# Kernel tuning notes

Hardware: AMD Instinct MI355X
Metric: run time of the kernel (lower is better)

The kernel has to match this reference:

```python
import jax, jax.numpy as jnp
import numpy as np

B, L, D, H, M = 4, 2048, 256, 8, 256
HEAD = D // H
EPS = 1e-6


def _pos_embedding(maxlen, d):
    i = np.arange(maxlen, dtype=np.float64)[:, None]
    j = np.arange(d, dtype=np.float64)[None, :]
    angle = i / np.power(10000.0, (j - (j % 2)) / d)
    pe = np.where(j % 2 == 0, np.sin(angle), np.cos(angle))
    return jnp.asarray(pe, jnp.float32)  # [L, D]


def _projection_matrix(m, d, seed=0):
    # FAVOR+ orthogonal random features: one full QR block (m == d here),
    # rows rescaled by norms of iid Gaussian rows (scaling=0 in source).
    rng = np.random.default_rng(seed)
    block = rng.standard_normal((d, d))
    q, _ = np.linalg.qr(block)
    q = q.T[:m]
    mult = np.linalg.norm(rng.standard_normal((m, d)), axis=1)
    return jnp.asarray(mult[:, None] * q, jnp.float32)  # [M, D]


def _softmax_kernel(x, is_query, proj):
    # x: [B, L, H, D], proj: [M, D]
    d = x.shape[-1]
    m = proj.shape[0]
    x = x * (float(d) ** -0.25)
    xp = jnp.einsum('blhd,md->blhm', x, proj)
    diag = 0.5 * jnp.sum(x * x, axis=-1, keepdims=True)
    if is_query:
        mx = jnp.max(xp, axis=-1, keepdims=True)
    else:
        mx = jnp.max(xp, axis=(-3, -1), keepdims=True)  # over L and M
    return (float(m) ** -0.5) * (jnp.exp(xp - diag - mx) + EPS)


def setup_inputs() -> dict:
    key = jax.random.key(0)
    ks = jax.random.split(key, 12)
    s = 1.0 / np.sqrt(D)
    inp = {
        'query': jax.random.normal(ks[0], (B, L, D), jnp.float32),
        'key': jax.random.normal(ks[1], (B, L, D), jnp.float32),
        'value': jax.random.normal(ks[2], (B, L, D), jnp.float32),
        'mask': jnp.ones((B, L), jnp.float32),
        'Wq': jax.random.normal(ks[3], (D, D), jnp.float32) * s,
        'bq': jnp.zeros((D,), jnp.float32),
        'Wk': jax.random.normal(ks[4], (D, D), jnp.float32) * s,
        'bk': jnp.zeros((D,), jnp.float32),
        'Wv': jax.random.normal(ks[5], (D, D), jnp.float32) * s,
        'bv': jnp.zeros((D,), jnp.float32),
        'Wo': jax.random.normal(ks[6], (D, D), jnp.float32) * s,
        'bo': jnp.zeros((D,), jnp.float32),
        'proj': _projection_matrix(M, D, seed=0),
        'pos': _pos_embedding(L, D),
    }
    return inp


def reference(query, key, value, mask, Wq, bq, Wk, bk, Wv, bv, Wo, bo, proj, pos):
    b = query.shape[0]
    q = query @ Wq + bq                      # [B, L, D]
    k = key @ Wk + bk
    v = value @ Wv + bv
    # per-head copies keep the FULL model_size feature dim (as in source)
    q = jnp.broadcast_to(q[:, :, None, :], (b, L, H, D))
    k = jnp.broadcast_to(k[:, :, None, :], (b, L, H, D))
    pos_b = pos[None]                        # [1, L, D]
    cos_pos = jnp.repeat(pos_b[..., None, 1::2], 2, axis=-1)  # [1, L, 1, D]
    sin_pos = jnp.repeat(pos_b[..., None, ::2], 2, axis=-1)

    def rot(x):
        x2 = jnp.stack([-x[..., 1::2], x[..., ::2]], axis=-1).reshape(x.shape)
        return x * cos_pos + x2 * sin_pos

    q = rot(q)
    k = rot(k)
    v = v.reshape(b, L, H, HEAD)

    qp = _softmax_kernel(q, True, proj)      # [B, L, H, M]
    kp = _softmax_kernel(k, False, proj)     # [B, L, H, M]

    kvs = jnp.einsum('blhm,blhd->bhmd', kp, v)
    num = jnp.einsum('blhm,bhmd->blhd', qp, kvs)
    den = jnp.einsum('blhm,bhm->blh', qp, jnp.sum(kp, axis=1))
    ctx = (num / den[..., None]).reshape(b, L, D)
    return ctx @ Wo + bo
```

## Files before the change

### kernel.cpp

```cpp
#include <hip/hip_runtime.h>

typedef unsigned short u16;
typedef unsigned int u32;
typedef __bf16 bf16x8 __attribute__((ext_vector_type(8)));
typedef float f32x4 __attribute__((ext_vector_type(4)));

__device__ __forceinline__ float bf2f(u16 u) { return __uint_as_float(((u32)u) << 16); }
__device__ __forceinline__ u16 f2bf(float f) {
  u32 x = __float_as_uint(f);
  x += 0x7fffu + ((x >> 16) & 1u);
  return (u16)(x >> 16);
}
__device__ __forceinline__ u32 encf(float x) {
  u32 u = __float_as_uint(x);
  return (u >> 31) ? ~u : (u | 0x80000000u);
}
__device__ __forceinline__ float decf(u32 e) {
  return (e >> 31) ? __uint_as_float(e & 0x7fffffffu) : __uint_as_float(~e);
}

#define MFMA(a, b, c) __builtin_amdgcn_mfma_f32_16x16x32_bf16(a, b, c, 0, 0, 0)

__global__ __launch_bounds__(256) void prep_w(
    const float* Wq, const float* Wk, const float* Wv, const float* Wo,
    const float* proj, const float* bv,
    u16* WqT, u16* WkT, u16* projb, u16* WWT, float* bw,
    float* __restrict__ ksum, u32* __restrict__ mxk) {
  __shared__ u16 tsh[32][33];
  __shared__ u16 As[64][40];
  __shared__ u16 Bs[64][40];
  const int z = blockIdx.z;
  const int x = threadIdx.x, y = threadIdx.y;
  const int tid = y * 32 + x;
  if (z < 2) {
    const float* s = z == 0 ? Wq : Wk;
    u16* d = z == 0 ? WqT : WkT;
    int r0 = blockIdx.y * 32, c0 = blockIdx.x * 32;
#pragma unroll
    for (int i = 0; i < 32; i += 8) tsh[y + i][x] = f2bf(s[(r0 + y + i) * 256 + c0 + x]);
    __syncthreads();
#pragma unroll
    for (int i = 0; i < 32; i += 8) d[(c0 + y + i) * 256 + r0 + x] = tsh[x][y + i];
    return;
  }
  if (z == 2) {
    int r0 = blockIdx.y * 32, c0 = blockIdx.x * 32;
#pragma unroll
    for (int i = 0; i < 32; i += 8)
      projb[(r0 + y + i) * 256 + c0 + x] = f2bf(proj[(r0 + y + i) * 256 + c0 + x]);
    return;
  }
  if (blockIdx.x < 4 && blockIdx.y < 4) {
    const int o0 = blockIdx.x * 64, i0 = blockIdx.y * 64;
    const int lane = tid & 63, wid = tid >> 6;
    const int wm = (wid >> 1) * 32, wn = (wid & 1) * 32;
    const int fm = lane & 15, fq = (lane >> 4) * 8, rowq = (lane >> 4) * 4;
    const int dr = tid >> 3, oc = (tid & 7) * 8;
    const int ir = tid >> 2, dc = (tid & 3) * 8;
    f32x4 acc[2][2] = {};
    for (int it = 0; it < 8; ++it) {
      int d0 = it * 32;
      float4 w0 = *(const float4*)(Wo + (d0 + dr) * 256 + o0 + oc);
      float4 w1 = *(const float4*)(Wo + (d0 + dr) * 256 + o0 + oc + 4);
      float4 v0 = *(const float4*)(Wv + (i0 + ir) * 256 + d0 + dc);
      float4 v1 = *(const float4*)(Wv + (i0 + ir) * 256 + d0 + dc + 4);
      __syncthreads();
      float wv[8] = {w0.x, w0.y, w0.z, w0.w, w1.x, w1.y, w1.z, w1.w};
#pragma unroll
      for (int j = 0; j < 8; ++j) As[oc + j][dr] = f2bf(wv[j]);
      u16* bp = &Bs[ir][dc];
      bp[0] = f2bf(v0.x); bp[1] = f2bf(v0.y); bp[2] = f2bf(v0.z); bp[3] = f2bf(v0.w);
      bp[4] = f2bf(v1.x); bp[5] = f2bf(v1.y); bp[6] = f2bf(v1.z); bp[7] = f2bf(v1.w);
      __syncthreads();
      bf16x8 a0 = *(const bf16x8*)&As[wm + fm][fq];
      bf16x8 a1 = *(const bf16x8*)&As[wm + 16 + fm][fq];
      bf16x8 b0 = *(const bf16x8*)&Bs[wn + fm][fq];
      bf16x8 b1 = *(const bf16x8*)&Bs[wn + 16 + fm][fq];
      acc[0][0] = MFMA(a0, b0, acc[0][0]);
      acc[0][1] = MFMA(a0, b1, acc[0][1]);
      acc[1][0] = MFMA(a1, b0, acc[1][0]);
      acc[1][1] = MFMA(a1, b1, acc[1][1]);
    }
#pragma unroll
    for (int mt = 0; mt < 2; ++mt)
#pragma unroll
      for (int nt = 0; nt < 2; ++nt)
#pragma unroll
        for (int r = 0; r < 4; ++r)
          WWT[(o0 + wm + mt * 16 + rowq + r) * 256 + i0 + wn + nt * 16 + fm] =
              f2bf(acc[mt][nt][r]);
    return;
  }
  if (blockIdx.x == 4 && blockIdx.y == 0) {
    float s = 0.0f;
    for (int d = 0; d < 256; ++d) s = fmaf(bv[d], Wo[d * 256 + tid], s);
    bw[tid] = s;
    for (int i = tid; i < 1024; i += 256) ksum[i] = 0.0f;
    if (tid < 4) mxk[tid] = 0u;
  }
}

__global__ __launch_bounds__(256, 3) void projrot2(
    const float* __restrict__ Xq, const float* __restrict__ Xk,
    const u16* __restrict__ WqT, const u16* __restrict__ WkT,
    const float* __restrict__ bq, const float* __restrict__ bk,
    const float* __restrict__ pos, const u16* __restrict__ projb,
    float* __restrict__ diag_k, u16* __restrict__ qp,
    float* __restrict__ xp, u32* __restrict__ mxk) {
  const int mode = blockIdx.z;
  const float* X = mode ? Xq : Xk;
  const u16* W = mode ? WqT : WkT;
  const float* bias = mode ? bq : bk;
  __shared__ u16 As[32][40];
  __shared__ u16 Bs[256][40];
  __shared__ u16 cbuf[32][264];
  __shared__ float dred[2][32];
  __shared__ float mred[2][32];
  __shared__ float wred[4];
  const int row0 = blockIdx.x * 32;
  const int t = threadIdx.x;
  const int lane = t & 63, wid = t >> 6;
  const int wrow = wid & 1, wcol = wid >> 1;
  const int fm = lane & 15, fq = (lane >> 4) * 8, rowq = (lane >> 4) * 4;
  const int ar = t >> 3, ak = (t & 7) * 4;

  f32x4 acc[8] = {};
  float4 av = *(const float4*)(X + (long long)(row0 + ar) * 256 + ak);
  uint4 bv0 = ((const uint4*)(W + (long long)t * 256))[0];
  uint4 bv1 = ((const uint4*)(W + (long long)t * 256))[1];
  uint4 bv2 = ((const uint4*)(W + (long long)t * 256))[2];
  uint4 bv3 = ((const uint4*)(W + (long long)t * 256))[3];
  for (int s = 0; s < 8; ++s) {
    __syncthreads();
    As[ar][ak] = f2bf(av.x); As[ar][ak + 1] = f2bf(av.y);
    As[ar][ak + 2] = f2bf(av.z); As[ar][ak + 3] = f2bf(av.w);
    uint4* bsp = (uint4*)&Bs[t][0];
    bsp[0] = bv0; bsp[1] = bv1; bsp[2] = bv2; bsp[3] = bv3;
    __syncthreads();
    if (s < 7) {
      const int k1 = (s + 1) * 32;
      av = *(const float4*)(X + (long long)(row0 + ar) * 256 + k1 + ak);
      const uint4* wn = (const uint4*)(W + (long long)t * 256 + k1);
      bv0 = wn[0]; bv1 = wn[1]; bv2 = wn[2]; bv3 = wn[3];
    }
    bf16x8 af = *(const bf16x8*)&As[wrow * 16 + fm][fq];
#pragma unroll
    for (int j = 0; j < 8; ++j) {
      bf16x8 bf = *(const bf16x8*)&Bs[wcol * 128 + j * 16 + fm][fq];
      acc[j] = MFMA(af, bf, acc[j]);
    }
  }

  float dsum[4] = {};
#pragma unroll
  for (int j = 0; j < 8; ++j) {
    float bb2 = bias[wcol * 128 + j * 16 + fm];
#pragma unroll
    for (int r = 0; r < 4; ++r) {
      float v = acc[j][r] + bb2;
      acc[j][r] = v;
      dsum[r] += v * v;
    }
  }
#pragma unroll
  for (int o = 1; o < 16; o <<= 1)
#pragma unroll
    for (int r = 0; r < 4; ++r) dsum[r] += __shfl_xor(dsum[r], o, 64);
  if (fm == 0) {
#pragma unroll
    for (int r = 0; r < 4; ++r) dred[wcol][wrow * 16 + rowq + r] = dsum[r];
  }
  __syncthreads();
  if (mode == 0 && t < 32) diag_k[row0 + t] = 0.03125f * (dred[0][t] + dred[1][t]);

#pragma unroll
  for (int j = 0; j < 8; ++j) {
    const int c = wcol * 128 + j * 16 + fm;
#pragma unroll
    for (int r = 0; r < 4; ++r) {
      const int row = wrow * 16 + rowq + r;
      const int l = (row0 + row) & 2047;
      float v = acc[j][r];
      float prt = __shfl_xor(v, 1, 64);
      float x2 = (fm & 1) ? prt : -prt;
      float2 cs = *(const float2*)(pos + (long long)l * 256 + (c & ~1));
      cbuf[row][c] = f2bf(0.25f * (v * cs.y + x2 * cs.x));
    }
  }

  f32x4 acc2[8] = {};
  uint4 pv0 = ((const uint4*)(projb + (long long)t * 256))[0];
  uint4 pv1 = ((const uint4*)(projb + (long long)t * 256))[1];
  uint4 pv2 = ((const uint4*)(projb + (long long)t * 256))[2];
  uint4 pv3 = ((const uint4*)(projb + (long long)t * 256))[3];
  for (int s = 0; s < 8; ++s) {
    __syncthreads();
    uint4* bsp = (uint4*)&Bs[t][0];
    bsp[0] = pv0; bsp[1] = pv1; bsp[2] = pv2; bsp[3] = pv3;
    __syncthreads();
    if (s < 7) {
      const uint4* pn = (const uint4*)(projb + (long long)t * 256 + (s + 1) * 32);
      pv0 = pn[0]; pv1 = pn[1]; pv2 = pn[2]; pv3 = pn[3];
    }
    bf16x8 af = *(const bf16x8*)&cbuf[wrow * 16 + fm][s * 32 + fq];
#pragma unroll
    for (int j = 0; j < 8; ++j) {
      bf16x8 bf = *(const bf16x8*)&Bs[wcol * 128 + j * 16 + fm][fq];
      acc2[j] = MFMA(af, bf, acc2[j]);
    }
  }

  if (mode == 1) {
    float m4[4] = {-3.0e38f, -3.0e38f, -3.0e38f, -3.0e38f};
#pragma unroll
    for (int j = 0; j < 8; ++j)
#pragma unroll
      for (int r = 0; r < 4; ++r) m4[r] = fmaxf(m4[r], acc2[j][r]);
#pragma unroll
    for (int o = 1; o < 16; o <<= 1)
#pragma unroll
      for (int r = 0; r < 4; ++r) m4[r] = fmaxf(m4[r], __shfl_xor(m4[r], o, 64));
    if (fm == 0) {
#pragma unroll
      for (int r = 0; r < 4; ++r) mred[wcol][wrow * 16 + rowq + r] = m4[r];
    }
    __syncthreads();
#pragma unroll
    for (int j = 0; j < 8; ++j) {
      const int col = wcol * 128 + j * 16 + fm;
#pragma unroll
      for (int r = 0; r < 4; ++r) {
        const int row = wrow * 16 + rowq + r;
        float mxr = fmaxf(mred[0][row], mred[1][row]);
        float dgr = 0.03125f * (dred[0][row] + dred[1][row]);
        float v = 0.0625f * (__expf(acc2[j][r] - dgr - mxr) + 1e-6f);
        qp[(long long)(row0 + row) * 256 + col] = f2bf(v);
      }
    }
  } else {
    float mx = -3.0e38f;
#pragma unroll
    for (int j = 0; j < 8; ++j) {
      int col = wcol * 128 + j * 16 + fm;
#pragma unroll
      for (int r = 0; r < 4; ++r) {
        float v = acc2[j][r];
        xp[(long long)(row0 + wrow * 16 + rowq + r) * 256 + col] = v;
        mx = fmaxf(mx, v);
      }
    }
#pragma unroll
    for (int o = 32; o > 0; o >>= 1) mx = fmaxf(mx, __shfl_xor(mx, o, 64));
    if (lane == 0) wred[wid] = mx;
    __syncthreads();
    if (t == 0) {
      float m = fmaxf(fmaxf(wred[0], wred[1]), fmaxf(wred[2], wred[3]));
      atomicMax(mxk + (row0 >> 11), encf(m));
    }
  }
}

__global__ __launch_bounds__(256, 2) void kvs_raw_split(
    const float* __restrict__ xp, const float* __restrict__ Xv,
    const float* __restrict__ diag_k, const u32* __restrict__ mxk,
    float* __restrict__ part, float* __restrict__ ksum) {
  __shared__ union USM {
    struct { u16 As[64][40]; u16 Bs[64][40]; } s;
    float ksbuf[32][65];
  } sm;
  const int mxt = blockIdx.x, ny = blockIdx.y, z = blockIdx.z;
  const int b = z >> 3, kc = z & 7;
  const long long l0 = (long long)b * 2048 + kc * 256;
  const int t = threadIdx.x;
  const int lane = t & 63, wid = t >> 6;
  const int wrow = wid >> 1, wcol = wid & 1;
  const int fm = lane & 15, fq = (lane >> 4) * 8, rowq = (lane >> 4) * 4;
  const float mxv = decf(mxk[b]);
  const int sr = t >> 3, sc = (t & 7) * 8;
  f32x4 acc[2][2] = {};
  float ksp[8] = {};
  long long lrow = l0 + sr;
  float4 x0 = *(const float4*)(xp + lrow * 256 + mxt * 64 + sc);
  float4 x1 = *(const float4*)(xp + lrow * 256 + mxt * 64 + sc + 4);
  float4 v0 = *(const float4*)(Xv + lrow * 256 + ny * 64 + sc);
  float4 v1 = *(const float4*)(Xv + lrow * 256 + ny * 64 + sc + 4);
  float dgl = diag_k[lrow];
  for (int s = 0; s < 8; ++s) {
    float xv[8] = {x0.x, x0.y, x0.z, x0.w, x1.x, x1.y, x1.z, x1.w};
    float vv[8] = {v0.x, v0.y, v0.z, v0.w, v1.x, v1.y, v1.z, v1.w};
    u16 kpv[8], vpv[8];
#pragma unroll
    for (int j = 0; j < 8; ++j) {
      float v = 0.0625f * (__expf(xv[j] - dgl - mxv) + 1e-6f);
      kpv[j] = f2bf(v);
      ksp[j] += bf2f(kpv[j]);
      vpv[j] = f2bf(vv[j]);
    }
    __syncthreads();
#pragma unroll
    for (int j = 0; j < 8; ++j) {
      sm.s.As[sc + j][sr] = kpv[j];
      sm.s.Bs[sc + j][sr] = vpv[j];
    }
    __syncthreads();
    if (s < 7) {
      lrow = l0 + (s + 1) * 32 + sr;
      x0 = *(const float4*)(xp + lrow * 256 + mxt * 64 + sc);
      x1 = *(const float4*)(xp + lrow * 256 + mxt * 64 + sc + 4);
      v0 = *(const float4*)(Xv + lrow * 256 + ny * 64 + sc);
      v1 = *(const float4*)(Xv + lrow * 256 + ny * 64 + sc + 4);
      dgl = diag_k[lrow];
    }
    bf16x8 a0 = *(const bf16x8*)&sm.s.As[wrow * 32 + fm][fq];
    bf16x8 a1 = *(const bf16x8*)&sm.s.As[wrow * 32 + 16 + fm][fq];
    bf16x8 b0 = *(const bf16x8*)&sm.s.Bs[wcol * 32 + fm][fq];
    bf16x8 b1 = *(const bf16x8*)&sm.s.Bs[wcol * 32 + 16 + fm][fq];
    acc[0][0] = MFMA(a0, b0, acc[0][0]);
    acc[0][1] = MFMA(a0, b1, acc[0][1]);
    acc[1][0] = MFMA(a1, b0, acc[1][0]);
    acc[1][1] = MFMA(a1, b1, acc[1][1]);
  }
#pragma unroll
  for (int mt = 0; mt < 2; ++mt)
#pragma unroll
    for (int nt = 0; nt < 2; ++nt)
#pragma unroll
      for (int r = 0; r < 4; ++r)
        part[(long long)z * 65536 +
             (long long)(mxt * 64 + wrow * 32 + mt * 16 + rowq + r) * 256 +
             ny * 64 + wcol * 32 + nt * 16 + fm] = acc[mt][nt][r];
  __syncthreads();
#pragma unroll
  for (int j = 0; j < 8; ++j) sm.ksbuf[sr][sc + j] = ksp[j];
  __syncthreads();
  if (ny == 0 && t < 64) {
    float ssum = 0.0f;
    for (int r = 0; r < 32; ++r) ssum += sm.ksbuf[r][t];
    atomicAdd(ksum + b * 256 + mxt * 64 + t, ssum);
  }
}

__global__ __launch_bounds__(256) void kvsw(
    const u16* __restrict__ WWT, const float* __restrict__ part,
    const float* __restrict__ ksum, const float* __restrict__ bw,
    u16* __restrict__ kvsWT) {
  __shared__ u16 As[64][40];
  __shared__ u16 Bs[16][40];
  const int bid = blockIdx.x;
  const int b = bid >> 6;
  const int o0 = ((bid >> 4) & 3) * 64;
  const int m0 = (bid & 15) * 16;
  const int t = threadIdx.x;
  const int w4 = t >> 6;
  const int lane = t & 63;
  const int fm = lane & 15, fq = (lane >> 4) * 8, rowq = (lane >> 4) * 4;
  const int arow = t >> 2, acol = (t & 3) * 8;
  const int brow = t >> 4, bcol = (t & 15) * 2;
  f32x4 acc = {0.0f, 0.0f, 0.0f, 0.0f};
  uint4 av = *(const uint4*)(WWT + (o0 + arow) * 256 + acol);
  float2 ps[8];
  {
    const float* pb = part + (long long)(b * 8) * 65536 + (m0 + brow) * 256 + bcol;
#pragma unroll
    for (int kc = 0; kc < 8; ++kc) ps[kc] = *(const float2*)(pb + (long long)kc * 65536);
  }
  for (int s = 0; s < 8; ++s) {
    float sx = ps[0].x + ps[1].x + ps[2].x + ps[3].x + ps[4].x + ps[5].x + ps[6].x + ps[7].x;
    float sy = ps[0].y + ps[1].y + ps[2].y + ps[3].y + ps[4].y + ps[5].y + ps[6].y + ps[7].y;
    __syncthreads();
    *(uint4*)&As[arow][acol] = av;
    Bs[brow][bcol] = f2bf(sx);
    Bs[brow][bcol + 1] = f2bf(sy);
    __syncthreads();
    if (s < 7) {
      const int k1 = (s + 1) * 32;
      av = *(const uint4*)(WWT + (o0 + arow) * 256 + k1 + acol);
      const float* pb = part + (long long)(b * 8) * 65536 + (m0 + brow) * 256 + k1 + bcol;
#pragma unroll
      for (int kc = 0; kc < 8; ++kc) ps[kc] = *(const float2*)(pb + (long long)kc * 65536);
    }
    bf16x8 af = *(const bf16x8*)&As[w4 * 16 + fm][fq];
    bf16x8 bf = *(const bf16x8*)&Bs[fm][fq];
    acc = MFMA(af, bf, acc);
  }
  const int col = m0 + fm;
  float ksv = ksum[b * 256 + col];
#pragma unroll
  for (int r = 0; r < 4; ++r) {
    int row = o0 + w4 * 16 + rowq + r;
    kvsWT[(long long)b * 65536 + (long long)row * 256 + col] =
        f2bf(acc[r] + bw[row] * ksv);
  }
}

__global__ __launch_bounds__(256, 4) void numout(
    const u16* __restrict__ qp, const float* __restrict__ ksum,
    const u16* __restrict__ kvsWT, const float* __restrict__ bo,
    float* __restrict__ out) {
  __shared__ u16 As[16][40];
  __shared__ u16 Bs[256][40];
  __shared__ float ksm[256], dsh[16];
  const int row0 = blockIdx.x * 16;
  const int b = blockIdx.z;
  const long long qrow = (long long)b * 2048 + row0;
  const int t = threadIdx.x;
  const int lane = t & 63, wid = t >> 6;
  const int fm = lane & 15, fq = (lane >> 4) * 8, rowq = (lane >> 4) * 4;
  const int ar = t >> 4, ak = (t & 15) * 2;

  u32 a0 = *(const u32*)(qp + (qrow + ar) * 256 + ak);
  const u16* kvr = kvsWT + (long long)b * 65536 + (long long)t * 256;
  uint4 bv0 = ((const uint4*)kvr)[0];
  uint4 bv1 = ((const uint4*)kvr)[1];
  uint4 bv2 = ((const uint4*)kvr)[2];
  uint4 bv3 = ((const uint4*)kvr)[3];

  ksm[t] = ksum[b * 256 + t];
  const int prow = t >> 4, pc0 = (t & 15) * 16;
  const u16* qr = qp + (qrow + prow) * 256 + pc0;
  uint4 u0 = *(const uint4*)(qr);
  uint4 u1 = *(const uint4*)(qr + 8);
  __syncthreads();

  float denp = 0.0f;
  u32 uu[8] = {u0.x, u0.y, u0.z, u0.w, u1.x, u1.y, u1.z, u1.w};
#pragma unroll
  for (int j = 0; j < 8; ++j) {
    denp += bf2f((u16)(uu[j] & 0xffffu)) * ksm[pc0 + 2 * j];
    denp += bf2f((u16)(uu[j] >> 16)) * ksm[pc0 + 2 * j + 1];
  }
#pragma unroll
  for (int o = 1; o < 16; o <<= 1) denp += __shfl_xor(denp, o, 64);
  if ((t & 15) == 0) dsh[prow] = denp;

  f32x4 acc[4] = {};
  for (int s = 0; s < 8; ++s) {
    __syncthreads();
    *(u32*)&As[ar][ak] = a0;
    uint4* bsp = (uint4*)&Bs[t][0];
    bsp[0] = bv0; bsp[1] = bv1; bsp[2] = bv2; bsp[3] = bv3;
    __syncthreads();
    if (s < 7) {
      const int k1 = (s + 1) * 32;
      a0 = *(const u32*)(qp + (qrow + ar) * 256 + k1 + ak);
      const uint4* kn = (const uint4*)(kvr + k1);
      bv0 = kn[0]; bv1 = kn[1]; bv2 = kn[2]; bv3 = kn[3];
    }
    bf16x8 af = *(const bf16x8*)&As[fm][fq];
#pragma unroll
    for (int j = 0; j < 4; ++j) {
      bf16x8 bf = *(const bf16x8*)&Bs[wid * 64 + j * 16 + fm][fq];
      acc[j] = MFMA(af, bf, acc[j]);
    }
  }
#pragma unroll
  for (int j = 0; j < 4; ++j) {
    int col = wid * 64 + j * 16 + fm;
    float bb2 = bo[col];
#pragma unroll
    for (int r = 0; r < 4; ++r) {
      int l = rowq + r;
      out[(qrow + l) * 256 + col] = acc[j][r] / dsh[l] + bb2;
    }
  }
}

extern "C" void kernel_launch(void* const* d_in, const int* in_sizes, int n_in,
                              void* d_out, int out_size, void* d_ws, size_t ws_size,
                              hipStream_t stream) {
  (void)in_sizes; (void)n_in; (void)out_size; (void)ws_size;
  const float* query = (const float*)d_in[0];
  const float* key = (const float*)d_in[1];
  const float* value = (const float*)d_in[2];
  const float* Wq = (const float*)d_in[4];
  const float* bq = (const float*)d_in[5];
  const float* Wk = (const float*)d_in[6];
  const float* bk = (const float*)d_in[7];
  const float* Wv = (const float*)d_in[8];
  const float* bv = (const float*)d_in[9];
  const float* Wo = (const float*)d_in[10];
  const float* bo = (const float*)d_in[11];
  const float* proj = (const float*)d_in[12];
  const float* pos = (const float*)d_in[13];

  char* w = (char*)d_ws;
  u16* qp = (u16*)(w);
  float* xp = (float*)(w + (4 << 20));
  float* part = (float*)(w + (12 << 20));
  u16* kvsWT = (u16*)(w + (20 << 20));
  u16* WqT = (u16*)(w + (21 << 20));
  u16* WkT = WqT + 65536;
  u16* projb = WkT + 65536;
  u16* WWT = projb + 65536;
  float* diag_k = (float*)(w + (22 << 20));
  float* ksum = diag_k + 8192;
  float* bw = ksum + 1024;
  u32* mxk = (u32*)(bw + 256);

  prep_w<<<dim3(8, 8, 4), dim3(32, 8), 0, stream>>>(Wq, Wk, Wv, Wo, proj, bv,
                                                    WqT, WkT, projb, WWT, bw,
                                                    ksum, mxk);
  projrot2<<<dim3(256, 1, 2), dim3(256), 0, stream>>>(
      query, key, WqT, WkT, bq, bk, pos, projb, diag_k, qp, xp, mxk);
  kvs_raw_split<<<dim3(4, 4, 32), dim3(256), 0, stream>>>(xp, value, diag_k, mxk,
                                                          part, ksum);
  kvsw<<<dim3(256), dim3(256), 0, stream>>>(WWT, part, ksum, bw, kvsWT);
  numout<<<dim3(128, 1, 4), dim3(256), 0, stream>>>(qp, ksum, kvsWT, bo,
                                                    (float*)d_out);
}
```

Measured before the change: 76.16 us.

## Double-buffer shared-memory tiles in projection and KV-state GEMM kernels

Converts the K-loop staging in projrot2 (both GEMM phases) and kvs_raw_split to double-buffered shared memory with a two-stage register prefetch. This cuts the per-step barriers from two to one and lets the MFMAs on the current tile overlap the global loads and LDS stores for the next. The cost is roughly double the shared memory and more live registers, so projrot2's launch bound drops from 3 to 2 blocks per CU and occupancy may fall.

```diff
diff --git a/kernel.cpp b/kernel.cpp
--- a/kernel.cpp
+++ b/kernel.cpp
@@ -100,7 +100,7 @@
   }
 }
 
-__global__ __launch_bounds__(256, 3) void projrot2(
+__global__ __launch_bounds__(256, 2) void projrot2(
     const float* __restrict__ Xq, const float* __restrict__ Xk,
     const u16* __restrict__ WqT, const u16* __restrict__ WkT,
     const float* __restrict__ bq, const float* __restrict__ bk,
@@ -111,8 +111,8 @@
   const float* X = mode ? Xq : Xk;
   const u16* W = mode ? WqT : WkT;
   const float* bias = mode ? bq : bk;
-  __shared__ u16 As[32][40];
-  __shared__ u16 Bs[256][40];
+  __shared__ u16 As[2][32][40];
+  __shared__ u16 Bs[2][256][40];
   __shared__ u16 cbuf[32][264];
   __shared__ float dred[2][32];
   __shared__ float mred[2][32];
@@ -124,30 +124,42 @@
   const int fm = lane & 15, fq = (lane >> 4) * 8, rowq = (lane >> 4) * 4;
   const int ar = t >> 3, ak = (t & 7) * 4;
 
+  const float* Xr = X + (long long)(row0 + ar) * 256;
+  const u16* Wr = W + (long long)t * 256;
+  float4 av = *(const float4*)(Xr + ak);
+  uint4 bv0 = ((const uint4*)Wr)[0];
+  uint4 bv1 = ((const uint4*)Wr)[1];
+  uint4 bv2 = ((const uint4*)Wr)[2];
+  uint4 bv3 = ((const uint4*)Wr)[3];
+  As[0][ar][ak] = f2bf(av.x); As[0][ar][ak + 1] = f2bf(av.y);
+  As[0][ar][ak + 2] = f2bf(av.z); As[0][ar][ak + 3] = f2bf(av.w);
+  { uint4* bsp = (uint4*)&Bs[0][t][0]; bsp[0] = bv0; bsp[1] = bv1; bsp[2] = bv2; bsp[3] = bv3; }
+  av = *(const float4*)(Xr + 32 + ak);
+  { const uint4* wn = (const uint4*)(Wr + 32); bv0 = wn[0]; bv1 = wn[1]; bv2 = wn[2]; bv3 = wn[3]; }
+  __syncthreads();
   f32x4 acc[8] = {};
-  float4 av = *(const float4*)(X + (long long)(row0 + ar) * 256 + ak);
-  uint4 bv0 = ((const uint4*)(W + (long long)t * 256))[0];
-  uint4 bv1 = ((const uint4*)(W + (long long)t * 256))[1];
-  uint4 bv2 = ((const uint4*)(W + (long long)t * 256))[2];
-  uint4 bv3 = ((const uint4*)(W + (long long)t * 256))[3];
   for (int s = 0; s < 8; ++s) {
-    __syncthreads();
-    As[ar][ak] = f2bf(av.x); As[ar][ak + 1] = f2bf(av.y);
-    As[ar][ak + 2] = f2bf(av.z); As[ar][ak + 3] = f2bf(av.w);
-    uint4* bsp = (uint4*)&Bs[t][0];
-    bsp[0] = bv0; bsp[1] = bv1; bsp[2] = bv2; bsp[3] = bv3;
-    __syncthreads();
+    const int cur = s & 1;
+    float4 av2; uint4 nb0, nb1, nb2, nb3;
+    if (s < 6) {
+      av2 = *(const float4*)(Xr + (s + 2) * 32 + ak);
+      const uint4* wn = (const uint4*)(Wr + (s + 2) * 32);
+      nb0 = wn[0]; nb1 = wn[1]; nb2 = wn[2]; nb3 = wn[3];
+    }
+    bf16x8 af = *(const bf16x8*)&As[cur][wrow * 16 + fm][fq];
+#pragma unroll
+    for (int j = 0; j < 8; ++j) {
+      bf16x8 bf = *(const bf16x8*)&Bs[cur][wcol * 128 + j * 16 + fm][fq];
+      acc[j] = MFMA(af, bf, acc[j]);
+    }
     if (s < 7) {
-      const int k1 = (s + 1) * 32;
-      av = *(const float4*)(X + (long long)(row0 + ar) * 256 + k1 + ak);
-      const uint4* wn = (const uint4*)(W + (long long)t * 256 + k1);
-      bv0 = wn[0]; bv1 = wn[1]; bv2 = wn[2]; bv3 = wn[3];
-    }
-    bf16x8 af = *(const bf16x8*)&As[wrow * 16 + fm][fq];
-#pragma unroll
-    for (int j = 0; j < 8; ++j) {
-      bf16x8 bf = *(const bf16x8*)&Bs[wcol * 128 + j * 16 + fm][fq];
-      acc[j] = MFMA(af, bf, acc[j]);
+      const int nxt = cur ^ 1;
+      As[nxt][ar][ak] = f2bf(av.x); As[nxt][ar][ak + 1] = f2bf(av.y);
+      As[nxt][ar][ak + 2] = f2bf(av.z); As[nxt][ar][ak + 3] = f2bf(av.w);
+      uint4* bsp = (uint4*)&Bs[nxt][t][0];
+      bsp[0] = bv0; bsp[1] = bv1; bsp[2] = bv2; bsp[3] = bv3;
+      if (s < 6) { av = av2; bv0 = nb0; bv1 = nb1; bv2 = nb2; bv3 = nb3; }
+      __syncthreads();
     }
   }
 
@@ -188,25 +200,34 @@
     }
   }
 
+  const u16* Pr = projb + (long long)t * 256;
+  uint4 pv0 = ((const uint4*)Pr)[0];
+  uint4 pv1 = ((const uint4*)Pr)[1];
+  uint4 pv2 = ((const uint4*)Pr)[2];
+  uint4 pv3 = ((const uint4*)Pr)[3];
+  { uint4* bsp = (uint4*)&Bs[0][t][0]; bsp[0] = pv0; bsp[1] = pv1; bsp[2] = pv2; bsp[3] = pv3; }
+  { const uint4* pn = (const uint4*)(Pr + 32); pv0 = pn[0]; pv1 = pn[1]; pv2 = pn[2]; pv3 = pn[3]; }
+  __syncthreads();
   f32x4 acc2[8] = {};
-  uint4 pv0 = ((const uint4*)(projb + (long long)t * 256))[0];
-  uint4 pv1 = ((const uint4*)(projb + (long long)t * 256))[1];
-  uint4 pv2 = ((const uint4*)(projb + (long long)t * 256))[2];
-  uint4 pv3 = ((const uint4*)(projb + (long long)t * 256))[3];
   for (int s = 0; s < 8; ++s) {
-    __syncthreads();
-    uint4* bsp = (uint4*)&Bs[t][0];
-    bsp[0] = pv0; bsp[1] = pv1; bsp[2] = pv2; bsp[3] = pv3;
-    __syncthreads();
+    const int cur = s & 1;
+    uint4 np0, np1, np2, np3;
+    if (s < 6) {
+      const uint4* pn = (const uint4*)(Pr + (s + 2) * 32);
+      np0 = pn[0]; np1 = pn[1]; np2 = pn[2]; np3 = pn[3];
+    }
+    bf16x8 af = *(const bf16x8*)&cbuf[wrow * 16 + fm][s * 32 + fq];
+#pragma unroll
+    for (int j = 0; j < 8; ++j) {
+      bf16x8 bf = *(const bf16x8*)&Bs[cur][wcol * 128 + j * 16 + fm][fq];
+      acc2[j] = MFMA(af, bf, acc2[j]);
+    }
     if (s < 7) {
-      const uint4* pn = (const uint4*)(projb + (long long)t * 256 + (s + 1) * 32);
-      pv0 = pn[0]; pv1 = pn[1]; pv2 = pn[2]; pv3 = pn[3];
-    }
-    bf16x8 af = *(const bf16x8*)&cbuf[wrow * 16 + fm][s * 32 + fq];
-#pragma unroll
-    for (int j = 0; j < 8; ++j) {
-      bf16x8 bf = *(const bf16x8*)&Bs[wcol * 128 + j * 16 + fm][fq];
-      acc2[j] = MFMA(af, bf, acc2[j]);
+      const int nxt = cur ^ 1;
+      uint4* bsp = (uint4*)&Bs[nxt][t][0];
+      bsp[0] = pv0; bsp[1] = pv1; bsp[2] = pv2; bsp[3] = pv3;
+      if (s < 6) { pv0 = np0; pv1 = np1; pv2 = np2; pv3 = np3; }
+      __syncthreads();
     }
   }
 
@@ -264,10 +285,9 @@
     const float* __restrict__ xp, const float* __restrict__ Xv,
     const float* __restrict__ diag_k, const u32* __restrict__ mxk,
     float* __restrict__ part, float* __restrict__ ksum) {
-  __shared__ union USM {
-    struct { u16 As[64][40]; u16 Bs[64][40]; } s;
-    float ksbuf[32][65];
-  } sm;
+  __shared__ u16 As[2][64][40];
+  __shared__ u16 Bs[2][64][40];
+  __shared__ float ksbuf[32][65];
   const int mxt = blockIdx.x, ny = blockIdx.y, z = blockIdx.z;
   const int b = z >> 3, kc = z & 7;
   const long long l0 = (long long)b * 2048 + kc * 256;
@@ -285,40 +305,59 @@
   float4 v0 = *(const float4*)(Xv + lrow * 256 + ny * 64 + sc);
   float4 v1 = *(const float4*)(Xv + lrow * 256 + ny * 64 + sc + 4);
   float dgl = diag_k[lrow];
-  for (int s = 0; s < 8; ++s) {
+  {
     float xv[8] = {x0.x, x0.y, x0.z, x0.w, x1.x, x1.y, x1.z, x1.w};
     float vv[8] = {v0.x, v0.y, v0.z, v0.w, v1.x, v1.y, v1.z, v1.w};
-    u16 kpv[8], vpv[8];
 #pragma unroll
     for (int j = 0; j < 8; ++j) {
-      float v = 0.0625f * (__expf(xv[j] - dgl - mxv) + 1e-6f);
-      kpv[j] = f2bf(v);
-      ksp[j] += bf2f(kpv[j]);
-      vpv[j] = f2bf(vv[j]);
-    }
-    __syncthreads();
-#pragma unroll
-    for (int j = 0; j < 8; ++j) {
-      sm.s.As[sc + j][sr] = kpv[j];
-      sm.s.Bs[sc + j][sr] = vpv[j];
-    }
-    __syncthreads();
-    if (s < 7) {
-      lrow = l0 + (s + 1) * 32 + sr;
-      x0 = *(const float4*)(xp + lrow * 256 + mxt * 64 + sc);
-      x1 = *(const float4*)(xp + lrow * 256 + mxt * 64 + sc + 4);
-      v0 = *(const float4*)(Xv + lrow * 256 + ny * 64 + sc);
-      v1 = *(const float4*)(Xv + lrow * 256 + ny * 64 + sc + 4);
-      dgl = diag_k[lrow];
-    }
-    bf16x8 a0 = *(const bf16x8*)&sm.s.As[wrow * 32 + fm][fq];
-    bf16x8 a1 = *(const bf16x8*)&sm.s.As[wrow * 32 + 16 + fm][fq];
-    bf16x8 b0 = *(const bf16x8*)&sm.s.Bs[wcol * 32 + fm][fq];
-    bf16x8 b1 = *(const bf16x8*)&sm.s.Bs[wcol * 32 + 16 + fm][fq];
+      float f = 0.0625f * (__expf(xv[j] - dgl - mxv) + 1e-6f);
+      u16 kb = f2bf(f);
+      As[0][sc + j][sr] = kb;
+      ksp[j] += bf2f(kb);
+      Bs[0][sc + j][sr] = f2bf(vv[j]);
+    }
+  }
+  lrow = l0 + 32 + sr;
+  x0 = *(const float4*)(xp + lrow * 256 + mxt * 64 + sc);
+  x1 = *(const float4*)(xp + lrow * 256 + mxt * 64 + sc + 4);
+  v0 = *(const float4*)(Xv + lrow * 256 + ny * 64 + sc);
+  v1 = *(const float4*)(Xv + lrow * 256 + ny * 64 + sc + 4);
+  dgl = diag_k[lrow];
+  __syncthreads();
+  for (int s = 0; s < 8; ++s) {
+    const int cur = s & 1;
+    float4 nx0, nx1, nv0, nv1; float ndg;
+    if (s < 6) {
+      long long lr2 = l0 + (s + 2) * 32 + sr;
+      nx0 = *(const float4*)(xp + lr2 * 256 + mxt * 64 + sc);
+      nx1 = *(const float4*)(xp + lr2 * 256 + mxt * 64 + sc + 4);
+      nv0 = *(const float4*)(Xv + lr2 * 256 + ny * 64 + sc);
+      nv1 = *(const float4*)(Xv + lr2 * 256 + ny * 64 + sc + 4);
+      ndg = diag_k[lr2];
+    }
+    bf16x8 a0 = *(const bf16x8*)&As[cur][wrow * 32 + fm][fq];
+    bf16x8 a1 = *(const bf16x8*)&As[cur][wrow * 32 + 16 + fm][fq];
+    bf16x8 b0 = *(const bf16x8*)&Bs[cur][wcol * 32 + fm][fq];
+    bf16x8 b1 = *(const bf16x8*)&Bs[cur][wcol * 32 + 16 + fm][fq];
     acc[0][0] = MFMA(a0, b0, acc[0][0]);
     acc[0][1] = MFMA(a0, b1, acc[0][1]);
     acc[1][0] = MFMA(a1, b0, acc[1][0]);
     acc[1][1] = MFMA(a1, b1, acc[1][1]);
+    if (s < 7) {
+      const int nxt = cur ^ 1;
+      float xv[8] = {x0.x, x0.y, x0.z, x0.w, x1.x, x1.y, x1.z, x1.w};
+      float vv[8] = {v0.x, v0.y, v0.z, v0.w, v1.x, v1.y, v1.z, v1.w};
+#pragma unroll
+      for (int j = 0; j < 8; ++j) {
+        float f = 0.0625f * (__expf(xv[j] - dgl - mxv) + 1e-6f);
+        u16 kb = f2bf(f);
+        As[nxt][sc + j][sr] = kb;
+        ksp[j] += bf2f(kb);
+        Bs[nxt][sc + j][sr] = f2bf(vv[j]);
+      }
+      if (s < 6) { x0 = nx0; x1 = nx1; v0 = nv0; v1 = nv1; dgl = ndg; }
+      __syncthreads();
+    }
   }
 #pragma unroll
   for (int mt = 0; mt < 2; ++mt)
@@ -329,13 +368,12 @@
         part[(long long)z * 65536 +
              (long long)(mxt * 64 + wrow * 32 + mt * 16 + rowq + r) * 256 +
              ny * 64 + wcol * 32 + nt * 16 + fm] = acc[mt][nt][r];
-  __syncthreads();
-#pragma unroll
-  for (int j = 0; j < 8; ++j) sm.ksbuf[sr][sc + j] = ksp[j];
+#pragma unroll
+  for (int j = 0; j < 8; ++j) ksbuf[sr][sc + j] = ksp[j];
   __syncthreads();
   if (ny == 0 && t < 64) {
     float ssum = 0.0f;
-    for (int r = 0; r < 32; ++r) ssum += sm.ksbuf[r][t];
+    for (int r = 0; r < 32; ++r) ssum += ksbuf[r][t];
     atomicAdd(ksum + b * 256 + mxt * 64 + t, ssum);
   }
 }
```

Result: faster. 71.04 us (-6.7%).
